# Kernel optimization log

Hardware: AMD Instinct MI355X
Metric: run time of the kernel (lower is better)

## Reference

```python
import jax, jax.numpy as jnp
import numpy as np

CLASS_EMBED_DIM = 128
TOPK = 64
EPS = float(np.finfo(float).eps)
ALPHA = 0.99


def setup_inputs() -> dict:
    key = jax.random.key(0)
    k1, k2, k3 = jax.random.split(key, 3)
    b, n, d = 16, 256, 640  # d = embed_dim + class_embed_dim
    embed_dim, inner_dim = 512, 512
    x = jax.random.normal(k1, (b, n, d), dtype=jnp.float32)
    # kaiming-normal style init: std = sqrt(2 / fan_in)
    std = (2.0 / embed_dim) ** 0.5
    Wq = jax.random.normal(k2, (embed_dim, inner_dim), dtype=jnp.float32) * std
    Wk = jax.random.normal(k3, (embed_dim, inner_dim), dtype=jnp.float32) * std
    alpha = jnp.float32(ALPHA)
    return {"x": x, "Wq": Wq, "Wk": Wk, "alpha": alpha}


def reference(x, Wq, Wk, alpha):
    b, n, d = x.shape
    xf = x.reshape(b * n, d)            # (N, embed+class)
    xe = xf[:, :-CLASS_EMBED_DIM]       # (N, embed)
    q = xe @ Wq                         # (N, inner)
    k = xe @ Wk                         # (N, inner)
    D = q.shape[1]
    # dots[i,j] = mean_d (q_i - k_j)^2, via expansion (avoids N x N x D tensor)
    q2 = jnp.sum(q * q, axis=1)
    k2 = jnp.sum(k * k, axis=1)
    dots = (q2[:, None] + k2[None, :] - 2.0 * (q @ k.T)) / D  # (N, N)
    N = dots.shape[0]
    _, idx = jax.lax.top_k(dots, TOPK)  # largest, matching torch.topk
    mask = jnp.zeros_like(dots).at[jnp.arange(N)[:, None], idx].set(1.0)
    mask = ((mask + mask.T) > 0).astype(jnp.float32)
    attn = dots * mask
    A = jnp.eye(N, dtype=dots.dtype) - alpha * attn + EPS
    out = jnp.linalg.inv(A) @ xf        # (N, d); to_v is identity
    return out.reshape(b, n, d)
```

## Files before the change

kernel.cpp:

```cpp
#include <hip/hip_runtime.h>
#include <float.h>

#define NN 4096
#define DD 640
#define DE 512
#define NB 16
#define OB 128
#define NOB (NN/OB)
#define SB 128
#define NSB (NN/SB)

static __device__ __forceinline__ float4 ldg4(const float* p) { return *(const float4*)p; }

__global__ __launch_bounds__(256) void proj_gemm(
    const float* __restrict__ xf, const float* __restrict__ Wq,
    const float* __restrict__ Wk, float* __restrict__ q, float* __restrict__ kk_)
{
  __shared__ float Xs[32][68], Qs[32][68], Ks[32][68];
  const int i0 = blockIdx.x * 64, c0 = blockIdx.y * 64;
  const int t = threadIdx.x, tr = t >> 4, tc = t & 15;
  float accq[4][4] = {}, acck[4][4] = {};
  for (int kb = 0; kb < DE; kb += 32) {
    {
      int m = t >> 3, k4 = (t & 7) << 2;
      float4 v0 = ldg4(xf + (size_t)(i0 + m) * DD + kb + k4);
      float4 v1 = ldg4(xf + (size_t)(i0 + m + 32) * DD + kb + k4);
      Xs[k4+0][m] = v0.x; Xs[k4+1][m] = v0.y; Xs[k4+2][m] = v0.z; Xs[k4+3][m] = v0.w;
      Xs[k4+0][m+32] = v1.x; Xs[k4+1][m+32] = v1.y; Xs[k4+2][m+32] = v1.z; Xs[k4+3][m+32] = v1.w;
    }
    {
      int kr = t >> 3, n8 = (t & 7) << 3;
      *(float4*)&Qs[kr][n8]   = ldg4(Wq + (size_t)(kb + kr) * DE + c0 + n8);
      *(float4*)&Qs[kr][n8+4] = ldg4(Wq + (size_t)(kb + kr) * DE + c0 + n8 + 4);
      *(float4*)&Ks[kr][n8]   = ldg4(Wk + (size_t)(kb + kr) * DE + c0 + n8);
      *(float4*)&Ks[kr][n8+4] = ldg4(Wk + (size_t)(kb + kr) * DE + c0 + n8 + 4);
    }
    __syncthreads();
    #pragma unroll
    for (int kkk = 0; kkk < 32; ++kkk) {
      float a[4], bq[4], bk[4];
      *(float4*)a  = *(const float4*)&Xs[kkk][tr << 2];
      *(float4*)bq = *(const float4*)&Qs[kkk][tc << 2];
      *(float4*)bk = *(const float4*)&Ks[kkk][tc << 2];
      #pragma unroll
      for (int r = 0; r < 4; ++r)
        #pragma unroll
        for (int c = 0; c < 4; ++c) { accq[r][c] += a[r]*bq[c]; acck[r][c] += a[r]*bk[c]; }
    }
    __syncthreads();
  }
  #pragma unroll
  for (int r = 0; r < 4; ++r) {
    float* qp = q   + (size_t)(i0 + (tr<<2) + r) * DE + c0 + (tc<<2);
    float* kp = kk_ + (size_t)(i0 + (tr<<2) + r) * DE + c0 + (tc<<2);
    *(float4*)qp = make_float4(accq[r][0], accq[r][1], accq[r][2], accq[r][3]);
    *(float4*)kp = make_float4(acck[r][0], acck[r][1], acck[r][2], acck[r][3]);
  }
}

__global__ __launch_bounds__(256) void rownorm(
    const float* __restrict__ q, const float* __restrict__ kk_,
    float* __restrict__ q2, float* __restrict__ k2)
{
  int w = (blockIdx.x * 256 + threadIdx.x) >> 6;
  int lane = threadIdx.x & 63;
  const float* src = (w < NN) ? q : kk_;
  int row = (w < NN) ? w : w - NN;
  const float* p = src + (size_t)row * DE;
  float s = 0.f;
  for (int c = lane; c < DE; c += 64) { float v = p[c]; s += v * v; }
  for (int off = 32; off; off >>= 1) s += __shfl_down(s, off);
  if (lane == 0) { if (w < NN) q2[row] = s; else k2[row] = s; }
}

__global__ __launch_bounds__(256) void dots_gemm(
    const float* __restrict__ q, const float* __restrict__ kk_,
    const float* __restrict__ q2, const float* __restrict__ k2,
    float* __restrict__ dots)
{
  __shared__ float Qs[32][68], Ks[32][68];
  const int i0 = blockIdx.x * 64, j0 = blockIdx.y * 64;
  const int t = threadIdx.x, tr = t >> 4, tc = t & 15;
  float acc[4][4] = {};
  for (int kb = 0; kb < DE; kb += 32) {
    int m = t >> 3, k4 = (t & 7) << 2;
    {
      float4 v0 = ldg4(q + (size_t)(i0 + m) * DE + kb + k4);
      float4 v1 = ldg4(q + (size_t)(i0 + m + 32) * DE + kb + k4);
      Qs[k4+0][m] = v0.x; Qs[k4+1][m] = v0.y; Qs[k4+2][m] = v0.z; Qs[k4+3][m] = v0.w;
      Qs[k4+0][m+32] = v1.x; Qs[k4+1][m+32] = v1.y; Qs[k4+2][m+32] = v1.z; Qs[k4+3][m+32] = v1.w;
    }
    {
      float4 v0 = ldg4(kk_ + (size_t)(j0 + m) * DE + kb + k4);
      float4 v1 = ldg4(kk_ + (size_t)(j0 + m + 32) * DE + kb + k4);
      Ks[k4+0][m] = v0.x; Ks[k4+1][m] = v0.y; Ks[k4+2][m] = v0.z; Ks[k4+3][m] = v0.w;
      Ks[k4+0][m+32] = v1.x; Ks[k4+1][m+32] = v1.y; Ks[k4+2][m+32] = v1.z; Ks[k4+3][m+32] = v1.w;
    }
    __syncthreads();
    #pragma unroll
    for (int kkk = 0; kkk < 32; ++kkk) {
      float a[4], b[4];
      *(float4*)a = *(const float4*)&Qs[kkk][tr << 2];
      *(float4*)b = *(const float4*)&Ks[kkk][tc << 2];
      #pragma unroll
      for (int r = 0; r < 4; ++r)
        #pragma unroll
        for (int c = 0; c < 4; ++c) acc[r][c] += a[r]*b[c];
    }
    __syncthreads();
  }
  const float inv = 1.0f / (float)DE;
  float k2v[4]; *(float4*)k2v = ldg4(k2 + j0 + (tc<<2));
  #pragma unroll
  for (int r = 0; r < 4; ++r) {
    float q2v = q2[i0 + (tr<<2) + r];
    float o[4];
    #pragma unroll
    for (int c = 0; c < 4; ++c) o[c] = (q2v + k2v[c] - 2.0f*acc[r][c]) * inv;
    *(float4*)(dots + (size_t)(i0 + (tr<<2) + r) * NN + j0 + (tc<<2)) =
        make_float4(o[0], o[1], o[2], o[3]);
  }
}

__global__ __launch_bounds__(256) void topk_bits(
    const float* __restrict__ dots, unsigned int* __restrict__ bits)
{
  __shared__ float row[NN];
  __shared__ unsigned int b[128];
  __shared__ float rv[4]; __shared__ int ri[4];
  const int i = blockIdx.x, t = threadIdx.x;
  const float* dr = dots + (size_t)i * NN;
  for (int c = t; c < NN; c += 256) row[c] = dr[c];
  if (t < 128) b[t] = 0u;
  __syncthreads();
  for (int it = 0; it < 64; ++it) {
    float bv = -FLT_MAX; int bi = NN;
    for (int c = t; c < NN; c += 256) { float v = row[c]; if (v > bv) { bv = v; bi = c; } }
    for (int off = 32; off; off >>= 1) {
      float ov = __shfl_down(bv, off); int oi = __shfl_down(bi, off);
      if (ov > bv || (ov == bv && oi < bi)) { bv = ov; bi = oi; }
    }
    if ((t & 63) == 0) { rv[t >> 6] = bv; ri[t >> 6] = bi; }
    __syncthreads();
    if (t == 0) {
      float fv = rv[0]; int fi = ri[0];
      for (int w = 1; w < 4; ++w)
        if (rv[w] > fv || (rv[w] == fv && ri[w] < fi)) { fv = rv[w]; fi = ri[w]; }
      b[fi >> 5] |= 1u << (fi & 31);
      row[fi] = -FLT_MAX;
    }
    __syncthreads();
  }
  if (t < 128) bits[(size_t)i * 128 + t] = b[t];
}

__global__ __launch_bounds__(256) void build_A(
    float* __restrict__ A, const unsigned int* __restrict__ bits,
    const float* __restrict__ alpha_p)
{
  int tid = blockIdx.x * 256 + threadIdx.x;
  int i = tid >> 10;
  int j4 = (tid & 1023) << 2;
  float alpha = alpha_p[0];
  float* p = A + (size_t)i * NN + j4;
  float4 d = *(float4*)p;
  unsigned int wrow = bits[(size_t)i * 128 + (j4 >> 5)];
  float dv[4] = {d.x, d.y, d.z, d.w}, o[4];
  #pragma unroll
  for (int u = 0; u < 4; ++u) {
    int j = j4 + u;
    unsigned int m1 = (wrow >> (j & 31)) & 1u;
    unsigned int m2 = (bits[(size_t)j * 128 + (i >> 5)] >> (i & 31)) & 1u;
    float base = (i == j) ? 1.0f : 0.0f;
    o[u] = base - ((m1 | m2) ? alpha * dv[u] : 0.0f);
  }
  *(float4*)p = make_float4(o[0], o[1], o[2], o[3]);
}

__global__ __launch_bounds__(1024) void lu_panel(
    float* __restrict__ A, int k0, int ok0, int* __restrict__ piv)
{
  const int t = threadIdx.x;
  const int M = NN - k0;
  float a[4][NB];
  __shared__ float bufA[NB], bufB[NB];
  __shared__ float rv[16]; __shared__ int ri[16];
  __shared__ int s_pr;
  __shared__ int piv_s[NB];
  __shared__ int sd[32], ss[32];
  __shared__ float l16[16][17];
  __shared__ float gbuf[32][112];

  #pragma unroll
  for (int i = 0; i < 4; ++i) {
    int r = t + (i << 10);
    if (r < M) {
      const float* src = A + (size_t)(k0 + r) * NN + k0;
      #pragma unroll
      for (int c4 = 0; c4 < NB; c4 += 4) {
        float4 v = ldg4(src + c4);
        a[i][c4] = v.x; a[i][c4+1] = v.y; a[i][c4+2] = v.z; a[i][c4+3] = v.w;
      }
    }
  }

  #pragma unroll
  for (int j = 0; j < NB; ++j) {
    float bv = -1.0f; int br = 1 << 30;
    #pragma unroll
    for (int i = 0; i < 4; ++i) {
      int r = t + (i << 10);
      if (r >= j && r < M) {
        float v = fabsf(a[i][j]);
        if (v > bv || (v == bv && r < br)) { bv = v; br = r; }
      }
    }
    for (int off = 32; off; off >>= 1) {
      float ov = __shfl_down(bv, off); int orr = __shfl_down(br, off);
      if (ov > bv || (ov == bv && orr < br)) { bv = ov; br = orr; }
    }
    if ((t & 63) == 0) { rv[t >> 6] = bv; ri[t >> 6] = br; }
    __syncthreads();
    if (t == 0) {
      float fv = rv[0]; int fr = ri[0];
      for (int w = 1; w < 16; ++w)
        if (rv[w] > fv || (rv[w] == fv && ri[w] < fr)) { fv = rv[w]; fr = ri[w]; }
      s_pr = fr; piv_s[j] = k0 + fr;
    }
    __syncthreads();
    const int pr = s_pr, prT = pr & 1023, prS = pr >> 10;
    if (t == prT) {
      #pragma unroll
      for (int i2 = 0; i2 < 4; ++i2) if (i2 == prS) {
        #pragma unroll
        for (int c = 0; c < NB; ++c) bufB[c] = a[i2][c];
      }
    }
    if (t == j) {
      #pragma unroll
      for (int c = 0; c < NB; ++c) bufA[c] = a[0][c];
    }
    __syncthreads();
    if (t == j) {
      #pragma unroll
      for (int c = 0; c < NB; ++c) a[0][c] = bufB[c];
    }
    if (t == prT) {
      #pragma unroll
      for (int i2 = 0; i2 < 4; ++i2) if (i2 == prS) {
        #pragma unroll
        for (int c = 0; c < NB; ++c) a[i2][c] = bufA[c];
      }
    }
    float rp = 1.0f / bufB[j];
    #pragma unroll
    for (int i = 0; i < 4; ++i) {
      int r = t + (i << 10);
      if (r > j && r < M) {
        float mlt = a[i][j] * rp;
        a[i][j] = mlt;
        #pragma unroll
        for (int c = j + 1; c < NB; ++c) a[i][c] -= mlt * bufB[c];
      }
    }
    __syncthreads();
  }

  #pragma unroll
  for (int i = 0; i < 4; ++i) {
    int r = t + (i << 10);
    if (r < M) {
      float* dst = A + (size_t)(k0 + r) * NN + k0;
      #pragma unroll
      for (int c4 = 0; c4 < NB; c4 += 4)
        *(float4*)(dst + c4) = make_float4(a[i][c4], a[i][c4+1], a[i][c4+2], a[i][c4+3]);
    }
  }
  if (t < NB) piv[k0 + t] = piv_s[t];

  if (t < 16) {
    #pragma unroll
    for (int c2 = 0; c2 < NB; ++c2) l16[t][c2] = a[0][c2];
  }

  if (t < 32) {
    int slotrow = (t < NB) ? (k0 + t) : -1;
    int content = slotrow;
    int next_ext = NB;
    for (int j = 0; j < NB; ++j) {
      int p = piv_s[j];
      unsigned long long mask = __ballot(slotrow == p);
      int bslot;
      if (mask) bslot = __ffsll((unsigned long long)mask) - 1;
      else {
        bslot = next_ext;
        if (t == next_ext) { slotrow = p; content = p; }
        next_ext++;
      }
      int srcl = (t == j) ? bslot : ((t == bslot) ? j : t);
      content = __shfl(content, srcl);
    }
    sd[t] = slotrow;
    ss[t] = content;
  }
  __syncthreads();

  const int p16 = k0 - ok0;
  for (int idx = t; idx < 32 * 112; idx += 1024) {
    int i = idx / 112, cc = idx - i * 112;
    if (sd[i] >= 0 && sd[i] != ss[i]) {
      int c = ok0 + (cc < p16 ? cc : cc + NB);
      gbuf[i][cc] = A[(size_t)ss[i] * NN + c];
    }
  }
  __syncthreads();
  for (int idx = t; idx < 32 * 112; idx += 1024) {
    int i = idx / 112, cc = idx - i * 112;
    if (sd[i] >= 0 && sd[i] != ss[i]) {
      int c = ok0 + (cc < p16 ? cc : cc + NB);
      A[(size_t)sd[i] * NN + c] = gbuf[i][cc];
    }
  }
  __syncthreads();

  const int w = ok0 + OB - (k0 + NB);
  if (t < w) {
    int c = k0 + NB + t;
    int cc = p16 + t;
    float x[16];
    #pragma unroll
    for (int i = 0; i < 16; ++i)
      x[i] = (ss[i] != sd[i]) ? gbuf[i][cc] : A[(size_t)(k0 + i) * NN + c];
    #pragma unroll
    for (int i = 1; i < 16; ++i)
      #pragma unroll
      for (int j = 0; j < i; ++j) x[i] -= l16[i][j] * x[j];
    #pragma unroll
    for (int i = 0; i < 16; ++i) A[(size_t)(k0 + i) * NN + c] = x[i];
  }
}

__global__ __launch_bounds__(128) void net_perm128(
    const int* __restrict__ piv_g, int ok0,
    int* __restrict__ nd, int* __restrict__ ns)
{
  __shared__ int slotrow[256], content[256];
  __shared__ int found, next_ext;
  const int t = threadIdx.x;
  slotrow[t] = ok0 + t;       content[t] = ok0 + t;
  slotrow[t + 128] = -1;      content[t + 128] = -1;
  if (t == 0) next_ext = 128;
  for (int j = 0; j < OB; ++j) {
    __syncthreads();
    int p = piv_g[ok0 + j];
    if (t == 0) found = (p < ok0 + OB) ? (p - ok0) : -1;
    __syncthreads();
    if (p >= ok0 + OB && slotrow[t + 128] == p) found = t + 128;
    __syncthreads();
    if (t == 0) {
      int s2 = found;
      if (s2 < 0) { s2 = next_ext++; slotrow[s2] = p; content[s2] = p; }
      int tmp = content[j]; content[j] = content[s2]; content[s2] = tmp;
    }
  }
  __syncthreads();
  nd[t] = slotrow[t];           ns[t] = content[t];
  nd[t + 128] = slotrow[t + 128]; ns[t + 128] = content[t + 128];
}

__global__ __launch_bounds__(256) void perm_copy_out(
    const float* __restrict__ A, float* __restrict__ T,
    const int* __restrict__ nd, const int* __restrict__ ns, int ok0)
{
  int s = blockIdx.y;
  int d = nd[s], sr = ns[s];
  if (d < 0 || d == sr) return;
  int c = blockIdx.x * 1024 + threadIdx.x * 4;
  if (c >= ok0 && c < ok0 + OB) return;
  *(float4*)(T + (size_t)s * NN + c) = ldg4(A + (size_t)sr * NN + c);
}

__global__ __launch_bounds__(256) void perm_copy_in(
    float* __restrict__ A, const float* __restrict__ T,
    const int* __restrict__ nd, const int* __restrict__ ns, int ok0)
{
  int s = blockIdx.y;
  int d = nd[s], sr = ns[s];
  if (d < 0 || d == sr) return;
  int c = blockIdx.x * 1024 + threadIdx.x * 4;
  if (c >= ok0 && c < ok0 + OB) return;
  *(float4*)(A + (size_t)d * NN + c) = ldg4(T + (size_t)s * NN + c);
}

__global__ __launch_bounds__(64) void trsm128L(float* __restrict__ A, int ok0)
{
  __shared__ float Ls[64][65];
  __shared__ float xs[64][132];
  const int t = threadIdx.x;
  const int c = ok0 + OB + blockIdx.x * 64 + t;
  for (int i = 0; i < 128; ++i) xs[t][i] = A[(size_t)(ok0 + i) * NN + c];
  for (int i = 0; i < 64; ++i) Ls[i][t] = A[(size_t)(ok0 + i) * NN + ok0 + t];
  __syncthreads();
  for (int i = 1; i < 64; ++i) {
    float s = 0.f;
    #pragma unroll 4
    for (int j = 0; j < i; ++j) s += Ls[i][j] * xs[t][j];
    xs[t][i] -= s;
  }
  __syncthreads();
  for (int i = 0; i < 64; ++i) Ls[i][t] = A[(size_t)(ok0 + 64 + i) * NN + ok0 + t];
  __syncthreads();
  for (int i = 0; i < 64; ++i) {
    float s = 0.f;
    #pragma unroll 4
    for (int j = 0; j < 64; ++j) s += Ls[i][j] * xs[t][j];
    xs[t][64 + i] -= s;
  }
  __syncthreads();
  for (int i = 0; i < 64; ++i) Ls[i][t] = A[(size_t)(ok0 + 64 + i) * NN + ok0 + 64 + t];
  __syncthreads();
  for (int i = 1; i < 64; ++i) {
    float s = 0.f;
    #pragma unroll 4
    for (int j = 0; j < i; ++j) s += Ls[i][j] * xs[t][64 + j];
    xs[t][64 + i] -= s;
  }
  for (int i = 0; i < 128; ++i) A[(size_t)(ok0 + i) * NN + c] = xs[t][i];
}

__global__ __launch_bounds__(256) void rank_update(
    float* __restrict__ C, int ldc,
    const float* __restrict__ Aop, int lda,
    const float* __restrict__ Bop, int ldb,
    int Mr, int Nc, int K)
{
  __shared__ float As[16][68], Bs[16][68];
  const int m0 = blockIdx.x * 64, n0 = blockIdx.y * 64;
  const int t = threadIdx.x, tr = t >> 4, tc = t & 15;
  const float4 z4 = make_float4(0.f, 0.f, 0.f, 0.f);
  float acc[4][4] = {};
  for (int kb = 0; kb < K; kb += 16) {
    {
      int m = t >> 2, k4 = (t & 3) << 2;
      float4 v0 = (m0 + m < Mr) ? ldg4(Aop + (size_t)(m0 + m) * lda + kb + k4) : z4;
      As[k4+0][m] = v0.x; As[k4+1][m] = v0.y; As[k4+2][m] = v0.z; As[k4+3][m] = v0.w;
    }
    {
      int kr = t >> 4, n4 = (t & 15) << 2;
      bool ok = (n0 + n4 < Nc);
      float4 w0 = ok ? ldg4(Bop + (size_t)(kb + kr) * ldb + n0 + n4) : z4;
      *(float4*)&Bs[kr][n4] = w0;
    }
    __syncthreads();
    #pragma unroll
    for (int kkk = 0; kkk < 16; ++kkk) {
      float a[4], b[4];
      *(float4*)a = *(const float4*)&As[kkk][tr << 2];
      *(float4*)b = *(const float4*)&Bs[kkk][tc << 2];
      #pragma unroll
      for (int r = 0; r < 4; ++r)
        #pragma unroll
        for (int c = 0; c < 4; ++c) acc[r][c] += a[r] * b[c];
    }
    __syncthreads();
  }
  #pragma unroll
  for (int r = 0; r < 4; ++r) {
    int m = m0 + (tr << 2) + r;
    int n = n0 + (tc << 2);
    if (m < Mr && n < Nc) {
      float* cp = C + (size_t)m * ldc + n;
      float4 cv = *(float4*)cp;
      cv.x -= acc[r][0]; cv.y -= acc[r][1]; cv.z -= acc[r][2]; cv.w -= acc[r][3];
      *(float4*)cp = cv;
    }
  }
}

__global__ __launch_bounds__(128) void inv_tri(
    const float* __restrict__ Ag, float* __restrict__ invT, int upper)
{
  __shared__ float xs[128][128];
  const int s = blockIdx.x, t = threadIdx.x;
  const size_t r0 = (size_t)s * SB;
  for (int i = 0; i < 128; ++i) xs[i][t] = 0.0f;
  const float* Tb = Ag + r0 * NN + r0;
  if (!upper) {
    xs[t][t] = 1.0f;
    for (int i = 1; i < 128; ++i) {
      float ssum = 0.f;
      for (int j = 0; j < i; ++j) ssum += Tb[(size_t)i * NN + j] * xs[j][t];
      if (i != t) xs[i][t] = -ssum;
    }
  } else {
    xs[t][t] = 1.0f / Tb[(size_t)t * NN + t];
    for (int i = 126; i >= 0; --i) {
      float ssum = 0.f;
      for (int j = i + 1; j < 128; ++j) ssum += Tb[(size_t)i * NN + j] * xs[j][t];
      if (i != t) xs[i][t] = -ssum / Tb[(size_t)i * NN + i];
    }
  }
  for (int i = 0; i < 128; ++i) invT[(size_t)s * SB * SB + (size_t)i * SB + t] = xs[i][t];
}

__global__ __launch_bounds__(1024) void perm_compose(
    const int* __restrict__ piv, int* __restrict__ idxp)
{
  __shared__ int pl[NN];
  const int t = threadIdx.x;
  for (int j = t; j < NN; j += 1024) pl[j] = piv[j];
  __syncthreads();
  int pos[4] = { t, t + 1024, t + 2048, t + 3072 };
  for (int j = NN - 1; j >= 0; --j) {
    int p = pl[j];
    #pragma unroll
    for (int u = 0; u < 4; ++u) {
      int r = t + (u << 10);
      if (j <= r) {
        if (pos[u] == j) pos[u] = p;
        else if (pos[u] == p) pos[u] = j;
      }
    }
  }
  #pragma unroll
  for (int u = 0; u < 4; ++u) idxp[t + (u << 10)] = pos[u];
}

__global__ __launch_bounds__(256) void gather_rows(
    const float* __restrict__ xf, const int* __restrict__ idxp, float* __restrict__ out)
{
  const int r = blockIdx.x, t = threadIdx.x;
  const int src = idxp[r];
  const float4* s = (const float4*)(xf + (size_t)src * DD);
  float4* d = (float4*)(out + (size_t)r * DD);
  for (int c = t; c < DD / 4; c += 256) d[c] = s[c];
}

__global__ __launch_bounds__(256) void diag_apply(
    float* __restrict__ B, const float* __restrict__ Minv, int r0)
{
  __shared__ float Bs[128][68];
  const int c0 = blockIdx.x * 64, t = threadIdx.x;
  #pragma unroll
  for (int v = 0; v < 8; ++v) {
    int id = t + v * 256;
    int k = id >> 4, c4 = (id & 15) << 2;
    *(float4*)&Bs[k][c4] = ldg4(B + (size_t)(r0 + k) * DD + c0 + c4);
  }
  __syncthreads();
  const int tr = t >> 4, tc = t & 15;
  float acc[8][4] = {};
  for (int k4 = 0; k4 < 128; k4 += 4) {
    float b0[4], b1[4], b2[4], b3[4];
    *(float4*)b0 = *(const float4*)&Bs[k4+0][tc << 2];
    *(float4*)b1 = *(const float4*)&Bs[k4+1][tc << 2];
    *(float4*)b2 = *(const float4*)&Bs[k4+2][tc << 2];
    *(float4*)b3 = *(const float4*)&Bs[k4+3][tc << 2];
    #pragma unroll
    for (int rr = 0; rr < 8; ++rr) {
      float m[4]; *(float4*)m = ldg4(Minv + (size_t)(tr*8 + rr) * SB + k4);
      #pragma unroll
      for (int c = 0; c < 4; ++c)
        acc[rr][c] += m[0]*b0[c] + m[1]*b1[c] + m[2]*b2[c] + m[3]*b3[c];
    }
  }
  #pragma unroll
  for (int rr = 0; rr < 8; ++rr)
    *(float4*)(B + (size_t)(r0 + tr*8 + rr) * DD + c0 + (tc << 2)) =
        make_float4(acc[rr][0], acc[rr][1], acc[rr][2], acc[rr][3]);
}

extern "C" void kernel_launch(void* const* d_in, const int* in_sizes, int n_in,
                              void* d_out, int out_size, void* d_ws, size_t ws_size,
                              hipStream_t stream)
{
  const float* xf    = (const float*)d_in[0];
  const float* Wq    = (const float*)d_in[1];
  const float* Wk    = (const float*)d_in[2];
  const float* alpha = (const float*)d_in[3];
  float* out = (float*)d_out;
  char* ws = (char*)d_ws;

  float* Amat = (float*)(ws);
  float* q    = (float*)(ws + 67108864ull);
  float* kbuf = (float*)(ws + 75497472ull);
  float* invL = (float*)(ws + 83886080ull);
  float* invU = (float*)(ws + 85983232ull);
  unsigned int* bits = (unsigned int*)(ws + 88080384ull);
  float* q2   = (float*)(ws + 90177536ull);
  float* k2   = (float*)(ws + 90193920ull);
  int* piv    = (int*)(ws + 90210304ull);
  int* idxp   = (int*)(ws + 90226688ull);
  int* nd     = (int*)(ws + 90243072ull);
  int* ns     = (int*)(ws + 90275840ull);
  float* Tbuf = q;

  proj_gemm<<<dim3(NN/64, DE/64), 256, 0, stream>>>(xf, Wq, Wk, q, kbuf);
  rownorm<<<2 * NN / 4, 256, 0, stream>>>(q, kbuf, q2, k2);
  dots_gemm<<<dim3(NN/64, NN/64), 256, 0, stream>>>(q, kbuf, q2, k2, Amat);
  topk_bits<<<NN, 256, 0, stream>>>(Amat, bits);
  build_A<<<NN * NN / 4 / 256, 256, 0, stream>>>(Amat, bits, alpha);

  for (int ob = 0; ob < NOB; ++ob) {
    const int ok0 = ob * OB;
    for (int p = 0; p < OB / NB; ++p) {
      const int k0 = ok0 + p * NB;
      lu_panel<<<1, 1024, 0, stream>>>(Amat, k0, ok0, piv);
      if (p < OB / NB - 1) {
        const int k1 = k0 + NB;
        const int w = ok0 + OB - k1;
        const int M2 = NN - k1;
        rank_update<<<dim3((M2 + 63) / 64, (w + 63) / 64), 256, 0, stream>>>(
            Amat + (size_t)k1 * NN + k1, NN,
            Amat + (size_t)k1 * NN + k0, NN,
            Amat + (size_t)k0 * NN + k1, NN,
            M2, w, NB);
      }
    }
    net_perm128<<<1, 128, 0, stream>>>(piv, ok0, nd, ns);
    perm_copy_out<<<dim3(NN / 1024, 256), 256, 0, stream>>>(Amat, Tbuf, nd, ns, ok0);
    perm_copy_in<<<dim3(NN / 1024, 256), 256, 0, stream>>>(Amat, Tbuf, nd, ns, ok0);
    const int b1 = ok0 + OB;
    const int M2 = NN - b1;
    if (M2 > 0) {
      trsm128L<<<M2 / 64, 64, 0, stream>>>(Amat, ok0);
      rank_update<<<dim3(M2 / 64, M2 / 64), 256, 0, stream>>>(
          Amat + (size_t)b1 * NN + b1, NN,
          Amat + (size_t)b1 * NN + ok0, NN,
          Amat + (size_t)ok0 * NN + b1, NN,
          M2, M2, OB);
    }
  }

  inv_tri<<<NSB, 128, 0, stream>>>(Amat, invL, 0);
  inv_tri<<<NSB, 128, 0, stream>>>(Amat, invU, 1);
  perm_compose<<<1, 1024, 0, stream>>>(piv, idxp);
  gather_rows<<<NN, 256, 0, stream>>>(xf, idxp, out);

  for (int s = 0; s < NSB; ++s) {
    int r0 = s * SB;
    diag_apply<<<DD / 64, 256, 0, stream>>>(out, invL + (size_t)s * SB * SB, r0);
    if (r0 + SB < NN) {
      int M2 = NN - r0 - SB;
      rank_update<<<dim3(M2 / 64, DD / 64), 256, 0, stream>>>(
          out + (size_t)(r0 + SB) * DD, DD,
          Amat + (size_t)(r0 + SB) * NN + r0, NN,
          out + (size_t)r0 * DD, DD,
          M2, DD, SB);
    }
  }
  for (int s = NSB - 1; s >= 0; --s) {
    int r0 = s * SB;
    diag_apply<<<DD / 64, 256, 0, stream>>>(out, invU + (size_t)s * SB * SB, r0);
    if (r0 > 0) {
      rank_update<<<dim3(r0 / 64, DD / 64), 256, 0, stream>>>(
          out, DD,
          Amat + r0, NN,
          out + (size_t)r0 * DD, DD,
          r0, DD, SB);
    }
  }
}
```

Baseline: 40.80 ms.

## Rework LU panel pivoting to avoid row swaps, shrink perm and tri-solve serial chains

The LU panel kernel now runs with 512 threads, holding 8 rows per thread. Pivot search uses a packed 64-bit key reduction with a single barrier per column. Instead of physically swapping rows inside the panel, the kernel marks pivot rows as done and permutes them on writeback. net_perm128 becomes a single-wavefront shuffle/ballot loop with no per-step barriers, and the triangular solves use four-way split accumulators to shorten dependency chains. The intent is to cut synchronisation and serial latency on the panel's critical path, at the cost of more complex permutation bookkeeping and slightly different summation order.

```diff
diff --git a/kernel.cpp b/kernel.cpp
--- a/kernel.cpp
+++ b/kernel.cpp
@@ -177,23 +177,25 @@
   *(float4*)p = make_float4(o[0], o[1], o[2], o[3]);
 }
 
-__global__ __launch_bounds__(1024) void lu_panel(
+__global__ __launch_bounds__(512, 2) void lu_panel(
     float* __restrict__ A, int k0, int ok0, int* __restrict__ piv)
 {
   const int t = threadIdx.x;
   const int M = NN - k0;
-  float a[4][NB];
-  __shared__ float bufA[NB], bufB[NB];
-  __shared__ float rv[16]; __shared__ int ri[16];
-  __shared__ int s_pr;
+  float a[8][NB];
+  __shared__ float l16[16][17];
+  __shared__ float s_rp;
+  __shared__ unsigned long long wkey[8];
   __shared__ int piv_s[NB];
+  __shared__ int piv_addr[NB];
   __shared__ int sd[32], ss[32];
-  __shared__ float l16[16][17];
   __shared__ float gbuf[32][112];
 
-  #pragma unroll
-  for (int i = 0; i < 4; ++i) {
-    int r = t + (i << 10);
+  int done = 0;
+
+  #pragma unroll
+  for (int i = 0; i < 8; ++i) {
+    int r = t + (i << 9);
     if (r < M) {
       const float* src = A + (size_t)(k0 + r) * NN + k0;
       #pragma unroll
@@ -206,107 +208,95 @@
 
   #pragma unroll
   for (int j = 0; j < NB; ++j) {
-    float bv = -1.0f; int br = 1 << 30;
-    #pragma unroll
-    for (int i = 0; i < 4; ++i) {
-      int r = t + (i << 10);
-      if (r >= j && r < M) {
-        float v = fabsf(a[i][j]);
-        if (v > bv || (v == bv && r < br)) { bv = v; br = r; }
+    unsigned long long key = 0ull;
+    #pragma unroll
+    for (int i = 0; i < 8; ++i) {
+      int r = t + (i << 9);
+      if (r < M && !(done & (1 << i))) {
+        unsigned int fb = __float_as_uint(fabsf(a[i][j]));
+        unsigned long long k2 = ((unsigned long long)fb << 32) |
+                                (unsigned long long)(0xFFFFFFFFu - (unsigned)r);
+        if (k2 > key) key = k2;
       }
     }
     for (int off = 32; off; off >>= 1) {
-      float ov = __shfl_down(bv, off); int orr = __shfl_down(br, off);
-      if (ov > bv || (ov == bv && orr < br)) { bv = ov; br = orr; }
-    }
-    if ((t & 63) == 0) { rv[t >> 6] = bv; ri[t >> 6] = br; }
-    __syncthreads();
-    if (t == 0) {
-      float fv = rv[0]; int fr = ri[0];
-      for (int w = 1; w < 16; ++w)
-        if (rv[w] > fv || (rv[w] == fv && ri[w] < fr)) { fv = rv[w]; fr = ri[w]; }
-      s_pr = fr; piv_s[j] = k0 + fr;
-    }
-    __syncthreads();
-    const int pr = s_pr, prT = pr & 1023, prS = pr >> 10;
-    if (t == prT) {
-      #pragma unroll
-      for (int i2 = 0; i2 < 4; ++i2) if (i2 == prS) {
+      unsigned long long o = __shfl_down(key, off);
+      if (o > key) key = o;
+    }
+    if ((t & 63) == 0) wkey[t >> 6] = key;
+    __syncthreads();
+    unsigned long long kmax = wkey[0];
+    #pragma unroll
+    for (int wv = 1; wv < 8; ++wv) if (wkey[wv] > kmax) kmax = wkey[wv];
+    const int prr = (int)(0xFFFFFFFFu - (unsigned)(kmax & 0xFFFFFFFFull));
+    #pragma unroll
+    for (int i = 0; i < 8; ++i) {
+      int r = t + (i << 9);
+      if (r == prr) {
         #pragma unroll
-        for (int c = 0; c < NB; ++c) bufB[c] = a[i2][c];
-      }
-    }
-    if (t == j) {
-      #pragma unroll
-      for (int c = 0; c < NB; ++c) bufA[c] = a[0][c];
-    }
-    __syncthreads();
-    if (t == j) {
-      #pragma unroll
-      for (int c = 0; c < NB; ++c) a[0][c] = bufB[c];
-    }
-    if (t == prT) {
-      #pragma unroll
-      for (int i2 = 0; i2 < 4; ++i2) if (i2 == prS) {
-        #pragma unroll
-        for (int c = 0; c < NB; ++c) a[i2][c] = bufA[c];
-      }
-    }
-    float rp = 1.0f / bufB[j];
-    #pragma unroll
-    for (int i = 0; i < 4; ++i) {
-      int r = t + (i << 10);
-      if (r > j && r < M) {
+        for (int c = 0; c < NB; ++c) l16[j][c] = a[i][c];
+        s_rp = 1.0f / a[i][j];
+        done |= (1 << i);
+      }
+    }
+    if (t == 0) piv_s[j] = k0 + prr;
+    __syncthreads();
+    const float rp = s_rp;
+    #pragma unroll
+    for (int i = 0; i < 8; ++i) {
+      int r = t + (i << 9);
+      if (r < M && !(done & (1 << i))) {
         float mlt = a[i][j] * rp;
         a[i][j] = mlt;
         #pragma unroll
-        for (int c = j + 1; c < NB; ++c) a[i][c] -= mlt * bufB[c];
-      }
-    }
-    __syncthreads();
-  }
-
-  #pragma unroll
-  for (int i = 0; i < 4; ++i) {
-    int r = t + (i << 10);
+        for (int c = j + 1; c < NB; ++c) a[i][c] -= mlt * l16[j][c];
+      }
+    }
+  }
+  __syncthreads();
+
+  if (t < 64) {
+    const int L = t;
+    int slotrow = (L < 16) ? (k0 + L) : -1;
+    int content = slotrow;
+    int next_ext = 16;
+    for (int j = 0; j < NB; ++j) {
+      int p = piv_s[j];
+      unsigned long long mask = __ballot(L < 32 && content == p);
+      int bslot;
+      if (mask) bslot = __ffsll(mask) - 1;
+      else {
+        bslot = next_ext;
+        if (L == next_ext) { slotrow = p; content = p; }
+        next_ext++;
+      }
+      int addr = __shfl(slotrow, bslot);
+      if (L == 0) piv_addr[j] = addr;
+      int srcl = (L == j) ? bslot : ((L == bslot) ? j : L);
+      content = __shfl(content, srcl);
+    }
+    if (L < 32) { sd[L] = slotrow; ss[L] = content; }
+  }
+  __syncthreads();
+
+  #pragma unroll
+  for (int i = 0; i < 8; ++i) {
+    int r = t + (i << 9);
     if (r < M) {
-      float* dst = A + (size_t)(k0 + r) * NN + k0;
+      int R = k0 + r;
+      int dst = R;
+      for (int sidx = 0; sidx < 32; ++sidx)
+        if (ss[sidx] == R) { dst = sd[sidx]; break; }
+      float* dstp = A + (size_t)dst * NN + k0;
       #pragma unroll
       for (int c4 = 0; c4 < NB; c4 += 4)
-        *(float4*)(dst + c4) = make_float4(a[i][c4], a[i][c4+1], a[i][c4+2], a[i][c4+3]);
-    }
-  }
-  if (t < NB) piv[k0 + t] = piv_s[t];
-
-  if (t < 16) {
-    #pragma unroll
-    for (int c2 = 0; c2 < NB; ++c2) l16[t][c2] = a[0][c2];
-  }
-
-  if (t < 32) {
-    int slotrow = (t < NB) ? (k0 + t) : -1;
-    int content = slotrow;
-    int next_ext = NB;
-    for (int j = 0; j < NB; ++j) {
-      int p = piv_s[j];
-      unsigned long long mask = __ballot(slotrow == p);
-      int bslot;
-      if (mask) bslot = __ffsll((unsigned long long)mask) - 1;
-      else {
-        bslot = next_ext;
-        if (t == next_ext) { slotrow = p; content = p; }
-        next_ext++;
-      }
-      int srcl = (t == j) ? bslot : ((t == bslot) ? j : t);
-      content = __shfl(content, srcl);
-    }
-    sd[t] = slotrow;
-    ss[t] = content;
-  }
-  __syncthreads();
+        *(float4*)(dstp + c4) = make_float4(a[i][c4], a[i][c4+1], a[i][c4+2], a[i][c4+3]);
+    }
+  }
+  if (t < NB) piv[k0 + t] = piv_addr[t];
 
   const int p16 = k0 - ok0;
-  for (int idx = t; idx < 32 * 112; idx += 1024) {
+  for (int idx = t; idx < 32 * 112; idx += 512) {
     int i = idx / 112, cc = idx - i * 112;
     if (sd[i] >= 0 && sd[i] != ss[i]) {
       int c = ok0 + (cc < p16 ? cc : cc + NB);
@@ -314,14 +304,13 @@
     }
   }
   __syncthreads();
-  for (int idx = t; idx < 32 * 112; idx += 1024) {
+  for (int idx = t; idx < 32 * 112; idx += 512) {
     int i = idx / 112, cc = idx - i * 112;
-    if (sd[i] >= 0 && sd[i] != ss[i]) {
+    if ((i >= 16 || cc < p16) && sd[i] >= 0 && sd[i] != ss[i]) {
       int c = ok0 + (cc < p16 ? cc : cc + NB);
       A[(size_t)sd[i] * NN + c] = gbuf[i][cc];
     }
   }
-  __syncthreads();
 
   const int w = ok0 + OB - (k0 + NB);
   if (t < w) {
@@ -340,32 +329,50 @@
   }
 }
 
-__global__ __launch_bounds__(128) void net_perm128(
+__global__ __launch_bounds__(64) void net_perm128(
     const int* __restrict__ piv_g, int ok0,
     int* __restrict__ nd, int* __restrict__ ns)
 {
-  __shared__ int slotrow[256], content[256];
-  __shared__ int found, next_ext;
-  const int t = threadIdx.x;
-  slotrow[t] = ok0 + t;       content[t] = ok0 + t;
-  slotrow[t + 128] = -1;      content[t + 128] = -1;
-  if (t == 0) next_ext = 128;
+  __shared__ int pl[OB];
+  const int L = threadIdx.x;
+  pl[L] = piv_g[ok0 + L];
+  pl[L + 64] = piv_g[ok0 + 64 + L];
+  __syncthreads();
+  int c0 = ok0 + L, c1 = ok0 + 64 + L, c2 = -1, c3 = -1;
+  int sr2 = -1, sr3 = -1;
+  int next_ext = 128;
   for (int j = 0; j < OB; ++j) {
-    __syncthreads();
-    int p = piv_g[ok0 + j];
-    if (t == 0) found = (p < ok0 + OB) ? (p - ok0) : -1;
-    __syncthreads();
-    if (p >= ok0 + OB && slotrow[t + 128] == p) found = t + 128;
-    __syncthreads();
-    if (t == 0) {
-      int s2 = found;
-      if (s2 < 0) { s2 = next_ext++; slotrow[s2] = p; content[s2] = p; }
-      int tmp = content[j]; content[j] = content[s2]; content[s2] = tmp;
-    }
-  }
-  __syncthreads();
-  nd[t] = slotrow[t];           ns[t] = content[t];
-  nd[t + 128] = slotrow[t + 128]; ns[t + 128] = content[t + 128];
+    int p = pl[j];
+    int s2;
+    if (p < ok0 + OB) s2 = p - ok0;
+    else {
+      unsigned long long m2 = __ballot(sr2 == p);
+      unsigned long long m3 = __ballot(sr3 == p);
+      if (m2) s2 = 128 + (__ffsll(m2) - 1);
+      else if (m3) s2 = 192 + (__ffsll(m3) - 1);
+      else {
+        s2 = next_ext;
+        if (s2 < 192) { if (L == s2 - 128) { sr2 = p; c2 = p; } }
+        else          { if (L == s2 - 192) { sr3 = p; c3 = p; } }
+        next_ext++;
+      }
+    }
+    int jp = j >> 6, jl = j & 63, sp = s2 >> 6, sl = s2 & 63;
+    int vj0 = __shfl(c0, jl), vj1 = __shfl(c1, jl);
+    int vj = (jp == 0) ? vj0 : vj1;
+    int vs0 = __shfl(c0, sl), vs1 = __shfl(c1, sl), vs2 = __shfl(c2, sl), vs3 = __shfl(c3, sl);
+    int vs = (sp == 0) ? vs0 : (sp == 1) ? vs1 : (sp == 2) ? vs2 : vs3;
+    if (jp == 0 && L == jl) c0 = vs;
+    if (jp == 1 && L == jl) c1 = vs;
+    if (sp == 0 && L == sl) c0 = vj;
+    if (sp == 1 && L == sl) c1 = vj;
+    if (sp == 2 && L == sl) c2 = vj;
+    if (sp == 3 && L == sl) c3 = vj;
+  }
+  nd[L] = ok0 + L;        ns[L] = c0;
+  nd[64 + L] = ok0 + 64 + L; ns[64 + L] = c1;
+  nd[128 + L] = sr2;      ns[128 + L] = c2;
+  nd[192 + L] = sr3;      ns[192 + L] = c3;
 }
 
 __global__ __launch_bounds__(256) void perm_copy_out(
@@ -395,35 +402,46 @@
 __global__ __launch_bounds__(64) void trsm128L(float* __restrict__ A, int ok0)
 {
   __shared__ float Ls[64][65];
-  __shared__ float xs[64][132];
+  __shared__ float xs[64][133];
   const int t = threadIdx.x;
   const int c = ok0 + OB + blockIdx.x * 64 + t;
   for (int i = 0; i < 128; ++i) xs[t][i] = A[(size_t)(ok0 + i) * NN + c];
   for (int i = 0; i < 64; ++i) Ls[i][t] = A[(size_t)(ok0 + i) * NN + ok0 + t];
   __syncthreads();
   for (int i = 1; i < 64; ++i) {
-    float s = 0.f;
+    float s0 = 0.f, s1 = 0.f, s2 = 0.f, s3 = 0.f;
+    int j = 0;
+    for (; j + 3 < i; j += 4) {
+      s0 += Ls[i][j+0] * xs[t][j+0]; s1 += Ls[i][j+1] * xs[t][j+1];
+      s2 += Ls[i][j+2] * xs[t][j+2]; s3 += Ls[i][j+3] * xs[t][j+3];
+    }
+    for (; j < i; ++j) s0 += Ls[i][j] * xs[t][j];
+    xs[t][i] -= (s0 + s1) + (s2 + s3);
+  }
+  __syncthreads();
+  for (int i = 0; i < 64; ++i) Ls[i][t] = A[(size_t)(ok0 + 64 + i) * NN + ok0 + t];
+  __syncthreads();
+  for (int i = 0; i < 64; ++i) {
+    float s0 = 0.f, s1 = 0.f, s2 = 0.f, s3 = 0.f;
     #pragma unroll 4
-    for (int j = 0; j < i; ++j) s += Ls[i][j] * xs[t][j];
-    xs[t][i] -= s;
-  }
-  __syncthreads();
-  for (int i = 0; i < 64; ++i) Ls[i][t] = A[(size_t)(ok0 + 64 + i) * NN + ok0 + t];
-  __syncthreads();
-  for (int i = 0; i < 64; ++i) {
-    float s = 0.f;
-    #pragma unroll 4
-    for (int j = 0; j < 64; ++j) s += Ls[i][j] * xs[t][j];
-    xs[t][64 + i] -= s;
+    for (int j = 0; j < 64; j += 4) {
+      s0 += Ls[i][j+0] * xs[t][j+0]; s1 += Ls[i][j+1] * xs[t][j+1];
+      s2 += Ls[i][j+2] * xs[t][j+2]; s3 += Ls[i][j+3] * xs[t][j+3];
+    }
+    xs[t][64 + i] -= (s0 + s1) + (s2 + s3);
   }
   __syncthreads();
   for (int i = 0; i < 64; ++i) Ls[i][t] = A[(size_t)(ok0 + 64 + i) * NN + ok0 + 64 + t];
   __syncthreads();
   for (int i = 1; i < 64; ++i) {
-    float s = 0.f;
-    #pragma unroll 4
-    for (int j = 0; j < i; ++j) s += Ls[i][j] * xs[t][64 + j];
-    xs[t][64 + i] -= s;
+    float s0 = 0.f, s1 = 0.f, s2 = 0.f, s3 = 0.f;
+    int j = 0;
+    for (; j + 3 < i; j += 4) {
+      s0 += Ls[i][j+0] * xs[t][64+j+0]; s1 += Ls[i][j+1] * xs[t][64+j+1];
+      s2 += Ls[i][j+2] * xs[t][64+j+2]; s3 += Ls[i][j+3] * xs[t][64+j+3];
+    }
+    for (; j < i; ++j) s0 += Ls[i][j] * xs[t][64+j];
+    xs[t][64 + i] -= (s0 + s1) + (s2 + s3);
   }
   for (int i = 0; i < 128; ++i) A[(size_t)(ok0 + i) * NN + c] = xs[t][i];
 }
@@ -488,15 +506,31 @@
   if (!upper) {
     xs[t][t] = 1.0f;
     for (int i = 1; i < 128; ++i) {
-      float ssum = 0.f;
-      for (int j = 0; j < i; ++j) ssum += Tb[(size_t)i * NN + j] * xs[j][t];
+      float s0 = 0.f, s1 = 0.f, s2 = 0.f, s3 = 0.f;
+      int j = 0;
+      for (; j + 3 < i; j += 4) {
+        s0 += Tb[(size_t)i * NN + j+0] * xs[j+0][t];
+        s1 += Tb[(size_t)i * NN + j+1] * xs[j+1][t];
+        s2 += Tb[(size_t)i * NN + j+2] * xs[j+2][t];
+        s3 += Tb[(size_t)i * NN + j+3] * xs[j+3][t];
+      }
+      for (; j < i; ++j) s0 += Tb[(size_t)i * NN + j] * xs[j][t];
+      float ssum = (s0 + s1) + (s2 + s3);
       if (i != t) xs[i][t] = -ssum;
     }
   } else {
     xs[t][t] = 1.0f / Tb[(size_t)t * NN + t];
     for (int i = 126; i >= 0; --i) {
-      float ssum = 0.f;
-      for (int j = i + 1; j < 128; ++j) ssum += Tb[(size_t)i * NN + j] * xs[j][t];
+      float s0 = 0.f, s1 = 0.f, s2 = 0.f, s3 = 0.f;
+      int j = i + 1;
+      for (; j + 3 < 128; j += 4) {
+        s0 += Tb[(size_t)i * NN + j+0] * xs[j+0][t];
+        s1 += Tb[(size_t)i * NN + j+1] * xs[j+1][t];
+        s2 += Tb[(size_t)i * NN + j+2] * xs[j+2][t];
+        s3 += Tb[(size_t)i * NN + j+3] * xs[j+3][t];
+      }
+      for (; j < 128; ++j) s0 += Tb[(size_t)i * NN + j] * xs[j][t];
+      float ssum = (s0 + s1) + (s2 + s3);
       if (i != t) xs[i][t] = -ssum / Tb[(size_t)i * NN + i];
     }
   }
@@ -605,7 +639,7 @@
     const int ok0 = ob * OB;
     for (int p = 0; p < OB / NB; ++p) {
       const int k0 = ok0 + p * NB;
-      lu_panel<<<1, 1024, 0, stream>>>(Amat, k0, ok0, piv);
+      lu_panel<<<1, 512, 0, stream>>>(Amat, k0, ok0, piv);
       if (p < OB / NB - 1) {
         const int k1 = k0 + NB;
         const int w = ok0 + OB - k1;
@@ -617,7 +651,7 @@
             M2, w, NB);
       }
     }
-    net_perm128<<<1, 128, 0, stream>>>(piv, ok0, nd, ns);
+    net_perm128<<<1, 64, 0, stream>>>(piv, ok0, nd, ns);
     perm_copy_out<<<dim3(NN / 1024, 256), 256, 0, stream>>>(Amat, Tbuf, nd, ns, ok0);
     perm_copy_in<<<dim3(NN / 1024, 256), 256, 0, stream>>>(Amat, Tbuf, nd, ns, ok0);
     const int b1 = ok0 + OB;
```

Result: slower. 45.50 ms (+11.5%).
